# Kernel tuning notes

Hardware: AMD Instinct MI355X
Metric: run time of the kernel (lower is better)

The kernel has to match this reference:

```python
import jax, jax.numpy as jnp
import numpy as np

NUM_HEADS = 16
HEAD_DIM = 128
ROTARY_DIM = 32  # head_dim * rotary_pct(0.25)
ROPE_BASE = 10000.0
SCALE = HEAD_DIM ** -0.5


def _rotate_half(x):
    x1, x2 = jnp.split(x, 2, axis=-1)
    return jnp.concatenate((-x2, x1), axis=-1)


def _rope_tables(seq_len, dtype):
    inv_freq = 1.0 / (ROPE_BASE ** (jnp.arange(0, ROTARY_DIM, 2, dtype=jnp.float32) / ROTARY_DIM))
    freqs = jnp.arange(seq_len, dtype=jnp.float32)[:, None] * inv_freq[None, :]  # [S, rd/2]
    emb = jnp.concatenate((freqs, freqs), axis=-1)  # [S, rd]
    return jnp.cos(emb).astype(dtype), jnp.sin(emb).astype(dtype)


def setup_inputs() -> dict:
    key = jax.random.key(0)
    k1, k2, k3 = jax.random.split(key, 3)
    B, S, H = 2, 2048, 2048
    hidden_states = jax.random.normal(k1, (B, S, H), dtype=jnp.float32)
    attention_mask = jnp.zeros((B, 1, S, S), dtype=jnp.float32)
    Wqkv = jax.random.normal(k2, (H, 3 * H), dtype=jnp.float32) * (H ** -0.5)
    Wout = jax.random.normal(k3, (H, H), dtype=jnp.float32) * (H ** -0.5)
    return {"hidden_states": hidden_states, "attention_mask": attention_mask,
            "Wqkv": Wqkv, "Wout": Wout}


def reference(hidden_states, attention_mask, Wqkv, Wout):
    B, S, H = hidden_states.shape
    qkv = jnp.einsum('bsh,hk->bsk', hidden_states, Wqkv)  # [B,S,3H]
    q, k, v = jnp.split(qkv, 3, axis=-1)

    def to_heads(x):
        return x.reshape(B, S, NUM_HEADS, HEAD_DIM).transpose(0, 2, 1, 3)  # [B,nh,S,hd]

    q, k, v = to_heads(q), to_heads(k), to_heads(v)

    cos, sin = _rope_tables(S, hidden_states.dtype)  # [S, ROTARY_DIM]
    cos = cos[None, None, :, :]
    sin = sin[None, None, :, :]

    def rope(x):
        xr = x[..., :ROTARY_DIM]
        xr = xr * cos + _rotate_half(xr) * sin
        return jnp.concatenate((xr, x[..., ROTARY_DIM:]), axis=-1)

    q, k = rope(q), rope(k)

    scores = jnp.einsum('bhqd,bhkd->bhqk', q, k) * SCALE + attention_mask
    probs = jax.nn.softmax(scores, axis=-1)  # dropout p=0 -> identity
    ctx = jnp.einsum('bhqk,bhkd->bhqd', probs, v)
    ctx = ctx.transpose(0, 2, 1, 3).reshape(B, S, H)
    return jnp.einsum('bsh,ho->bso', ctx, Wout)
```

## Files before the change

### kernel.cpp

```cpp
#include <hip/hip_runtime.h>

typedef __attribute__((ext_vector_type(4))) float f32x4;
typedef __attribute__((ext_vector_type(8))) short s16x8;
typedef __attribute__((ext_vector_type(4))) unsigned short u16x4;
typedef __attribute__((ext_vector_type(8))) unsigned short u16x8;

#define DEVINL __device__ __forceinline__

constexpr int Bb = 2;
constexpr int Ss = 2048;
constexpr int Hh = 2048;
constexpr int NH = 16;
constexpr int HD = 128;
constexpr float ATT_SCALE = 0.08838834764831845f;
constexpr float CEXP = ATT_SCALE * 1.44269504089f;
constexpr float INV_SCALE = 11.313708498984761f;
constexpr float RAW_THR = 90.50966799f;

DEVINL unsigned short f2bf(float f) {
    unsigned u = __float_as_uint(f);
    u += 0x7FFFu + ((u >> 16) & 1u);
    return (unsigned short)(u >> 16);
}
DEVINL float bf2f(unsigned short h) { return __uint_as_float(((unsigned)h) << 16); }
DEVINL float fexp2(float x) { return __builtin_amdgcn_exp2f(x); }

DEVINL void gl16(const void* g, void* l) {
    __builtin_amdgcn_global_load_lds((const __attribute__((address_space(1))) void*)g,
                                     (__attribute__((address_space(3))) void*)l, 16, 0, 0);
}

__global__ void zero_flag_k(int* f) { if (threadIdx.x == 0) *f = 0; }

__global__ void scan_mask_k(const float* __restrict__ m, int* __restrict__ flag) {
    size_t i = ((size_t)blockIdx.x * 256 + threadIdx.x) * 4;
    f32x4 v = *(const f32x4*)(m + i);
    int any = (v[0] != 0.f) || (v[1] != 0.f) || (v[2] != 0.f) || (v[3] != 0.f);
    if (__any(any)) { if ((threadIdx.x & 63) == 0) atomicOr(flag, 1); }
}

__global__ void convH_k(const float* __restrict__ x, unsigned short* __restrict__ y) {
    size_t i = (size_t)blockIdx.x * 256 + threadIdx.x;
    f32x4 a = *(const f32x4*)(x + i * 8);
    f32x4 b = *(const f32x4*)(x + i * 8 + 4);
    u16x8 o;
    o[0] = f2bf(a[0]); o[1] = f2bf(a[1]); o[2] = f2bf(a[2]); o[3] = f2bf(a[3]);
    o[4] = f2bf(b[0]); o[5] = f2bf(b[1]); o[6] = f2bf(b[2]); o[7] = f2bf(b[3]);
    *(u16x8*)(y + i * 8) = o;
}

__global__ void convT_k(const float* __restrict__ W, unsigned short* __restrict__ Wt,
                        int R, int C) {
    __shared__ float tile[32][33];
    int c0 = blockIdx.x * 32, r0 = blockIdx.y * 32;
    int t = threadIdx.x;
    int rr = t >> 3, cc = (t & 7) * 4;
    f32x4 v = *(const f32x4*)(W + (size_t)(r0 + rr) * C + c0 + cc);
    tile[rr][cc + 0] = v[0]; tile[rr][cc + 1] = v[1];
    tile[rr][cc + 2] = v[2]; tile[rr][cc + 3] = v[3];
    __syncthreads();
    u16x4 o;
    o[0] = f2bf(tile[cc + 0][rr]); o[1] = f2bf(tile[cc + 1][rr]);
    o[2] = f2bf(tile[cc + 2][rr]); o[3] = f2bf(tile[cc + 3][rr]);
    *(u16x4*)(Wt + (size_t)(c0 + rr) * R + r0 + cc) = o;
}

#define PH(buf, kh, ih, sbuf, sunit, st, vm)                                      \
  {                                                                               \
    const char* Ar = lds + (buf)*65536;                                           \
    const char* Br = Ar + 32768;                                                  \
    s16x8 af[4];                                                                  \
    if ((ih) == 0) {                                                              \
      _Pragma("unroll")                                                           \
      for (int j = 0; j < 4; ++j) {                                               \
        int row = wn*64 + j*16 + lr;                                              \
        bfr[j] = *(const s16x8*)(Br + row*128 + (((kh)*64 + lg*16) ^ ((row&7)<<4))); \
      }                                                                           \
    }                                                                             \
    _Pragma("unroll")                                                             \
    for (int i = 0; i < 4; ++i) {                                                 \
      int row = wm*128 + (ih)*64 + i*16 + lr;                                     \
      af[i] = *(const s16x8*)(Ar + row*128 + (((kh)*64 + lg*16) ^ ((row&7)<<4))); \
    }                                                                             \
    STG(sbuf, sunit, st);                                                         \
    __builtin_amdgcn_s_barrier();                                                 \
    asm volatile("s_waitcnt lgkmcnt(0)" ::: "memory");                            \
    __builtin_amdgcn_s_setprio(1);                                                \
    _Pragma("unroll")                                                             \
    for (int i = 0; i < 4; ++i)                                                   \
      _Pragma("unroll")                                                           \
      for (int j = 0; j < 4; ++j)                                                 \
        acc[(ih)*4 + i][j] = __builtin_amdgcn_mfma_f32_16x16x32_bf16(             \
            af[i], bfr[j], acc[(ih)*4 + i][j], 0, 0, 0);                          \
    __builtin_amdgcn_s_setprio(0);                                                \
    if ((vm) == 2) { asm volatile("s_waitcnt vmcnt(2)" ::: "memory"); }           \
    if ((vm) == 4) { asm volatile("s_waitcnt vmcnt(4)" ::: "memory"); }           \
    __builtin_amdgcn_s_barrier();                                                 \
  }

template<int MODE>
__global__ __launch_bounds__(512, 2)
void gemm256_k(const unsigned short* __restrict__ A, const unsigned short* __restrict__ Bt,
               float* __restrict__ Cf, unsigned short* __restrict__ Cb,
               int M, int N, int K) {
    __shared__ char lds[131072];
    int t = threadIdx.x, w = t >> 6, ln = t & 63, lr = ln & 15, lg = ln >> 4;
    int wm = w >> 2, wn = w & 3;
    int f = blockIdx.x, cpx = gridDim.x >> 3;
    int s = (f & 7) * cpx + (f >> 3);
    int nbn = N >> 8;
    int nb = s % nbn, mb = s / nbn;
    int m0 = mb * 256, n0 = nb * 256;
    const char* Ab = (const char*)A;
    const char* Bbp = (const char*)Bt;

    f32x4 acc[8][4];
#pragma unroll
    for (int i = 0; i < 8; ++i)
#pragma unroll
        for (int j = 0; j < 4; ++j) { acc[i][j][0] = 0.f; acc[i][j][1] = 0.f; acc[i][j][2] = 0.f; acc[i][j][3] = 0.f; }

    auto STG = [&](int sbuf, int unit, int kt) {
        int isB = unit >> 1;
        const char* src = isB ? Bbp : Ab;
        int rbase = isB ? n0 : m0;
        char* reg = lds + sbuf * 65536 + isB * 32768;
        size_t kb = ((size_t)kt * 64) * 2;
#pragma unroll
        for (int rr = 0; rr < 2; ++rr) {
            int rowbase = isB ? ((unit & 1) * 128 + rr * 64)
                              : (rr * 128 + (unit & 1) * 64);
            int row = rowbase + (t >> 3);
            int slot = (t & 7) ^ (row & 7);
            gl16(src + ((size_t)(rbase + row) * K) * 2 + kb + slot * 16,
                 reg + rowbase * 128 + t * 16);
        }
    };

    const int NT = K >> 6;
    STG(0, 0, 0); STG(0, 2, 0); STG(0, 3, 0); STG(0, 1, 0);
    STG(1, 0, 1);
    asm volatile("s_waitcnt vmcnt(2)" ::: "memory");
    __builtin_amdgcn_s_barrier();

    s16x8 bfr[4];
    for (int it = 0; it < (NT >> 1); ++it) {
        int e = it * 2;
        int e2 = (e + 2 < NT) ? e + 2 : e;
        int e3 = (e + 3 < NT) ? e + 3 : e + 1;
        PH(0, 0, 0,  1, 2, e + 1, 4)
        PH(0, 0, 1,  1, 3, e + 1, -1)
        PH(0, 1, 0,  1, 1, e + 1, -1)
        PH(0, 1, 1,  0, 0, e2,    4)
        PH(1, 0, 0,  0, 2, e2,    4)
        PH(1, 0, 1,  0, 3, e2,   -1)
        PH(1, 1, 0,  0, 1, e2,   -1)
        PH(1, 1, 1,  1, 0, e3,    4)
    }
    asm volatile("s_waitcnt vmcnt(0)" ::: "memory");

    if (MODE == 0 && n0 < 4096 && (wn & 1) == 0) {
        float invf = fexp2((float)lr * -0.83048202372f);
#pragma unroll
        for (int i = 0; i < 8; ++i)
#pragma unroll
            for (int r = 0; r < 4; ++r) {
                int srow = (m0 + wm * 128 + i * 16 + lg * 4 + r) & (Ss - 1);
                float sn, cs;
                sincosf((float)srow * invf, &sn, &cs);
                float x1 = acc[i][0][r], x2 = acc[i][1][r];
                acc[i][0][r] = x1 * cs - x2 * sn;
                acc[i][1][r] = x2 * cs + x1 * sn;
            }
    }

#pragma unroll
    for (int i = 0; i < 8; ++i)
#pragma unroll
        for (int j = 0; j < 4; ++j)
#pragma unroll
            for (int r = 0; r < 4; ++r) {
                int gr = m0 + wm * 128 + i * 16 + lg * 4 + r;
                int gc = n0 + wn * 64 + j * 16 + lr;
                float vv = acc[i][j][r];
                if (MODE == 1) Cf[(size_t)gr * N + gc] = vv;
                else           Cb[(size_t)gr * N + gc] = f2bf(vv);
            }
}

template<int MODE>
__global__ __launch_bounds__(256)
void gemm_bt_k(const unsigned short* __restrict__ A, const unsigned short* __restrict__ Bt,
               float* __restrict__ Cf, unsigned short* __restrict__ Cb,
               int M, int N, int K) {
    __shared__ char lds[128 * 64 * 2 * 2];
    char* As = lds;
    char* Bs = lds + 128 * 64 * 2;
    int t = threadIdx.x, w = t >> 6, ln = t & 63, lr = ln & 15, lg = ln >> 4;
    int f = blockIdx.x;
    int cpx = gridDim.x >> 3;
    int s = (f & 7) * cpx + (f >> 3);
    int nbn = N >> 7;
    int nb = s % nbn, mb = s / nbn;
    int m0 = mb * 128, n0 = nb * 128;
    int wr = w >> 1, wc = w & 1;
    const char* Abt = (const char*)A;
    const char* Bbt = (const char*)Bt;

    f32x4 acc[4][4];
#pragma unroll
    for (int i = 0; i < 4; ++i)
#pragma unroll
        for (int j = 0; j < 4; ++j) { acc[i][j][0] = 0.f; acc[i][j][1] = 0.f; acc[i][j][2] = 0.f; acc[i][j][3] = 0.f; }

    for (int k0 = 0; k0 < K; k0 += 64) {
        __syncthreads();
#pragma unroll
        for (int vv = 0; vv < 4; ++vv) {
            int ci = vv * 256 + t;
            int row = ci >> 3, cb = (ci & 7) << 4;
            int sc = cb ^ ((row & 7) << 4);
            gl16(Abt + ((size_t)(m0 + row) * K + k0) * 2 + sc, As + ci * 16);
            gl16(Bbt + ((size_t)(n0 + row) * K + k0) * 2 + sc, Bs + ci * 16);
        }
        __syncthreads();
#pragma unroll
        for (int kc = 0; kc < 2; ++kc) {
            s16x8 af[4], bfr[4];
#pragma unroll
            for (int i = 0; i < 4; ++i) {
                int rowa = wr * 64 + i * 16 + lr;
                af[i] = *(const s16x8*)(As + rowa * 128 + ((kc * 64 + lg * 16) ^ ((rowa & 7) << 4)));
                int rowb = wc * 64 + i * 16 + lr;
                bfr[i] = *(const s16x8*)(Bs + rowb * 128 + ((kc * 64 + lg * 16) ^ ((rowb & 7) << 4)));
            }
#pragma unroll
            for (int i = 0; i < 4; ++i)
#pragma unroll
                for (int j = 0; j < 4; ++j)
                    acc[i][j] = __builtin_amdgcn_mfma_f32_16x16x32_bf16(af[i], bfr[j], acc[i][j], 0, 0, 0);
        }
    }
#pragma unroll
    for (int i = 0; i < 4; ++i)
#pragma unroll
        for (int j = 0; j < 4; ++j)
#pragma unroll
            for (int r = 0; r < 4; ++r) {
                int gr = m0 + wr * 64 + i * 16 + lg * 4 + r;
                int gc = n0 + wc * 64 + j * 16 + lr;
                float vv = acc[i][j][r];
                if (MODE == 1) Cf[(size_t)gr * N + gc] = vv;
                else           Cb[(size_t)gr * N + gc] = f2bf(vv);
            }
}

__global__ void vtrans_k(const unsigned short* __restrict__ qkv, unsigned short* __restrict__ Vt) {
    __shared__ unsigned short tile[64][40];
    int bh = blockIdx.x; int b = bh >> 4, h = bh & 15;
    int s0 = blockIdx.y * 64, d0 = blockIdx.z * 32;
    int t = threadIdx.x;
    int r = t >> 2, c8 = (t & 3) * 8;
    u16x8 v = *(const u16x8*)(qkv + ((size_t)(b * Ss + s0 + r)) * 6144 + 4096 + h * 128 + d0 + c8);
#pragma unroll
    for (int e = 0; e < 8; ++e) tile[r][c8 + e] = v[e];
    __syncthreads();
    int dr = t >> 3, sc = (t & 7) * 8;
    u16x8 o;
#pragma unroll
    for (int e = 0; e < 8; ++e) o[e] = tile[sc + e][dr];
    *(u16x8*)(Vt + ((size_t)bh * HD + d0 + dr) * Ss + s0 + sc) = o;
}

__global__ __launch_bounds__(512)
void attn_k(const unsigned short* __restrict__ qkv, const unsigned short* __restrict__ Vt,
            const float* __restrict__ mask, unsigned short* __restrict__ ctxb,
            const int* __restrict__ flag) {
    __shared__ char ldsK[2][16384];
    __shared__ char ldsV[2][16384];
    __shared__ unsigned short ldsP[8][1024];
    int f = blockIdx.x;
    int swzb = (f & 7) * 64 + (f >> 3);
    int bh = swzb >> 4, qt = swzb & 15;
    int b = bh >> 4, h = bh & 15;
    int t = threadIdx.x, w = t >> 6, ln = t & 63, lr = ln & 15, lg = ln >> 4;
    int useMask = *flag;
    int qw0 = qt * 128 + w * 16;
    const char* qkvB = (const char*)qkv;
    const char* VtB = (const char*)Vt;

    auto STAGE = [&](int buf, int kk0s) {
#pragma unroll
        for (int c = 0; c < 2; ++c) {
            int ci = c * 512 + t;
            int krow = ci >> 4, kcb = (ci & 15) << 4;
            gl16(qkvB + (((size_t)(b * Ss + kk0s + krow)) * 6144 + 2048 + h * 128) * 2 + (kcb ^ ((krow & 7) << 4)),
                 ldsK[buf] + ci * 16);
            int vrow = ci >> 3, vcb = (ci & 7) << 4;
            gl16(VtB + (((size_t)(bh * 128 + vrow)) * 2048 + kk0s) * 2 + (vcb ^ ((vrow & 7) << 4)),
                 ldsV[buf] + ci * 16);
        }
    };

    s16x8 qf[4];
    size_t qbase = ((size_t)(b * Ss + qw0 + lr)) * 6144 + h * 128;
#pragma unroll
    for (int kc = 0; kc < 4; ++kc) qf[kc] = *(const s16x8*)(qkv + qbase + kc * 32 + lg * 8);

    float mr = -3e38f, lsum = 0.f;
    f32x4 ctxa[8];
#pragma unroll
    for (int dn = 0; dn < 8; ++dn) { ctxa[dn][0] = 0.f; ctxa[dn][1] = 0.f; ctxa[dn][2] = 0.f; ctxa[dn][3] = 0.f; }
    const float* mrow = mask + (size_t)b * Ss * Ss;

    STAGE(0, 0);
    asm volatile("s_waitcnt vmcnt(0)" ::: "memory");
    __builtin_amdgcn_s_barrier();

    for (int tix = 0; tix < 32; ++tix) {
        int kk0 = tix * 64;
        int cur = tix & 1;
        if (kk0 + 64 < Ss) STAGE(cur ^ 1, kk0 + 64);

        f32x4 st[4];
#pragma unroll
        for (int n = 0; n < 4; ++n) {
            f32x4 sacc = {0.f, 0.f, 0.f, 0.f};
            const char* kb = ldsK[cur] + (n * 16 + lr) * 256;
            int sw = (lr & 7) << 4;
            s16x8 kf0 = *(const s16x8*)(kb + ((0 * 64 + lg * 16) ^ sw));
            s16x8 kf1 = *(const s16x8*)(kb + ((1 * 64 + lg * 16) ^ sw));
            s16x8 kf2 = *(const s16x8*)(kb + ((2 * 64 + lg * 16) ^ sw));
            s16x8 kf3 = *(const s16x8*)(kb + ((3 * 64 + lg * 16) ^ sw));
            __builtin_amdgcn_s_setprio(1);
            sacc = __builtin_amdgcn_mfma_f32_16x16x32_bf16(kf0, qf[0], sacc, 0, 0, 0);
            sacc = __builtin_amdgcn_mfma_f32_16x16x32_bf16(kf1, qf[1], sacc, 0, 0, 0);
            sacc = __builtin_amdgcn_mfma_f32_16x16x32_bf16(kf2, qf[2], sacc, 0, 0, 0);
            sacc = __builtin_amdgcn_mfma_f32_16x16x32_bf16(kf3, qf[3], sacc, 0, 0, 0);
            __builtin_amdgcn_s_setprio(0);
            st[n] = sacc;
        }
        if (useMask) {
#pragma unroll
            for (int n = 0; n < 4; ++n)
#pragma unroll
                for (int r = 0; r < 4; ++r)
                    st[n][r] += mrow[(size_t)(qw0 + lr) * Ss + kk0 + n * 16 + lg * 4 + r] * INV_SCALE;
        }
        float pmax = st[0][0];
#pragma unroll
        for (int n = 0; n < 4; ++n)
#pragma unroll
            for (int r = 0; r < 4; ++r) pmax = fmaxf(pmax, st[n][r]);
        pmax = fmaxf(pmax, __shfl_xor(pmax, 16));
        pmax = fmaxf(pmax, __shfl_xor(pmax, 32));
        bool need = pmax > mr + RAW_THR;
        if (__any(need)) {
            float mn = fmaxf(mr, pmax);
            float al = fexp2((mr - mn) * CEXP);
            mr = mn;
            lsum *= al;
            float a0 = __shfl(al, lg * 4 + 0), a1 = __shfl(al, lg * 4 + 1);
            float a2 = __shfl(al, lg * 4 + 2), a3 = __shfl(al, lg * 4 + 3);
#pragma unroll
            for (int dn = 0; dn < 8; ++dn) {
                ctxa[dn][0] *= a0; ctxa[dn][1] *= a1; ctxa[dn][2] *= a2; ctxa[dn][3] *= a3;
            }
        }
        float mC = mr * CEXP;
        float rs = 0.f;
        u16x4 pk[4];
#pragma unroll
        for (int n = 0; n < 4; ++n)
#pragma unroll
            for (int r = 0; r < 4; ++r) {
                float p = fexp2(st[n][r] * CEXP - mC);
                rs += p;
                pk[n][r] = f2bf(p);
            }
        rs += __shfl_xor(rs, 16);
        rs += __shfl_xor(rs, 32);
        lsum += rs;
        char* pw = (char*)ldsP[w];
        int swp = (lr & 7) << 4;
#pragma unroll
        for (int n = 0; n < 4; ++n)
            *(u16x4*)(pw + lr * 128 + ((32 * n + 8 * lg) ^ swp)) = pk[n];
        asm volatile("s_waitcnt lgkmcnt(0)" ::: "memory");
        s16x8 pa[2];
#pragma unroll
        for (int c2 = 0; c2 < 2; ++c2)
            pa[c2] = *(const s16x8*)(pw + lr * 128 + ((64 * c2 + 16 * lg) ^ swp));
#pragma unroll
        for (int dn = 0; dn < 8; ++dn) {
            const char* vb = ldsV[cur] + (dn * 16 + lr) * 128;
            s16x8 vf0 = *(const s16x8*)(vb + ((0 * 64 + lg * 16) ^ swp));
            s16x8 vf1 = *(const s16x8*)(vb + ((1 * 64 + lg * 16) ^ swp));
            __builtin_amdgcn_s_setprio(1);
            ctxa[dn] = __builtin_amdgcn_mfma_f32_16x16x32_bf16(pa[0], vf0, ctxa[dn], 0, 0, 0);
            ctxa[dn] = __builtin_amdgcn_mfma_f32_16x16x32_bf16(pa[1], vf1, ctxa[dn], 0, 0, 0);
            __builtin_amdgcn_s_setprio(0);
        }
        asm volatile("s_waitcnt vmcnt(0)" ::: "memory");
        __builtin_amdgcn_s_barrier();
    }
    float l0 = 1.f / __shfl(lsum, lg * 4 + 0), l1 = 1.f / __shfl(lsum, lg * 4 + 1);
    float l2 = 1.f / __shfl(lsum, lg * 4 + 2), l3 = 1.f / __shfl(lsum, lg * 4 + 3);
#pragma unroll
    for (int dn = 0; dn < 8; ++dn) {
        size_t base = ((size_t)(b * Ss + qw0)) * Hh + h * 128 + dn * 16 + lr;
        ctxb[base + (size_t)(lg * 4 + 0) * Hh] = f2bf(ctxa[dn][0] * l0);
        ctxb[base + (size_t)(lg * 4 + 1) * Hh] = f2bf(ctxa[dn][1] * l1);
        ctxb[base + (size_t)(lg * 4 + 2) * Hh] = f2bf(ctxa[dn][2] * l2);
        ctxb[base + (size_t)(lg * 4 + 3) * Hh] = f2bf(ctxa[dn][3] * l3);
    }
}

extern "C" void kernel_launch(void* const* d_in, const int* in_sizes, int n_in,
                              void* d_out, int out_size, void* d_ws, size_t ws_size,
                              hipStream_t stream) {
    (void)in_sizes; (void)n_in; (void)out_size; (void)ws_size;
    const float* hidden = (const float*)d_in[0];
    const float* mask   = (const float*)d_in[1];
    const float* Wqkv   = (const float*)d_in[2];
    const float* Wout   = (const float*)d_in[3];
    float* out = (float*)d_out;

    char* ws = (char*)d_ws;
    size_t off = 0;
    auto alloc = [&](size_t bytes) { char* p = ws + off; off += (bytes + 255) & ~(size_t)255; return p; };
    unsigned short* hbf   = (unsigned short*)alloc((size_t)8388608 * 2);
    unsigned short* wqkvT = (unsigned short*)alloc((size_t)12582912 * 2);
    unsigned short* woutT = (unsigned short*)alloc((size_t)4194304 * 2);
    unsigned short* qkv   = (unsigned short*)alloc((size_t)25165824 * 2);
    unsigned short* Vt    = (unsigned short*)alloc((size_t)8388608 * 2);
    int* flag             = (int*)alloc(256);
    unsigned short* ctx = hbf;

    zero_flag_k<<<1, 64, 0, stream>>>(flag);
    scan_mask_k<<<2048, 256, 0, stream>>>(mask, flag);
    convH_k<<<4096, 256, 0, stream>>>(hidden, hbf);
    convT_k<<<dim3(192, 64), 256, 0, stream>>>(Wqkv, wqkvT, 2048, 6144);
    convT_k<<<dim3(64, 64), 256, 0, stream>>>(Wout, woutT, 2048, 2048);
    gemm256_k<0><<<384, 512, 0, stream>>>(hbf, wqkvT, nullptr, qkv, 4096, 6144, 2048);
    vtrans_k<<<dim3(32, 32, 4), 256, 0, stream>>>(qkv, Vt);
    attn_k<<<512, 512, 0, stream>>>(qkv, Vt, mask, ctx, flag);
    gemm_bt_k<1><<<512, 256, 0, stream>>>(ctx, woutT, out, nullptr, 4096, 2048, 2048);
}
```

Measured before the change: 309.0 us.

## Replace both GEMMs with a pipelined 128x256-tile kernel using half-K LDS stages

Replaces the 256x256 QKV GEMM and the simple 128x128 output-projection GEMM with a single 128x256-tile kernel. Its LDS layout splits each K tile into 32-wide halves with a new XOR swizzle and keeps a double-buffered, barrier-phased prefetch schedule. The QKV GEMM now launches 768 blocks instead of 384, which improves occupancy and load balance on the many CUs, at the cost of less operand reuse per block. The output projection gains software pipelining but drops from 512 to 256 blocks.

```diff
diff --git a/kernel.cpp b/kernel.cpp
--- a/kernel.cpp
+++ b/kernel.cpp
@@ -65,24 +65,61 @@
     *(u16x4*)(Wt + (size_t)(c0 + rr) * R + r0 + cc) = o;
 }
 
-#define PH(buf, kh, ih, sbuf, sunit, st, vm)                                      \
+template<int MODE>
+__global__ __launch_bounds__(512, 2)
+void gemm128x256_k(const unsigned short* __restrict__ A, const unsigned short* __restrict__ Bt,
+                   float* __restrict__ Cf, unsigned short* __restrict__ Cb,
+                   int M, int N, int K) {
+    __shared__ char lds[98304];
+    int t = threadIdx.x, w = t >> 6, ln = t & 63, lr = ln & 15, lg = ln >> 4;
+    int wm = w >> 2, wn = w & 3;
+    int f = blockIdx.x, cpx = gridDim.x >> 3;
+    int s = (f & 7) * cpx + (f >> 3);
+    int nbn = N >> 8;
+    int nb = s % nbn, mb = s / nbn;
+    int m0 = mb * 128, n0 = nb * 256;
+    const char* Ab = (const char*)A;
+    const char* Bbp = (const char*)Bt;
+
+    f32x4 acc[4][4];
+#pragma unroll
+    for (int i = 0; i < 4; ++i)
+#pragma unroll
+        for (int j = 0; j < 4; ++j) { acc[i][j][0] = 0.f; acc[i][j][1] = 0.f; acc[i][j][2] = 0.f; acc[i][j][3] = 0.f; }
+
+    auto STGA = [&](int sbuf, int skh, int kt) {
+        int row = t >> 2, c = t & 3;
+        int cs = c ^ ((row >> 1) & 3);
+        gl16(Ab + ((size_t)(m0 + row) * K + kt * 64 + skh * 32) * 2 + cs * 16,
+             lds + sbuf * 49152 + skh * 8192 + t * 16);
+    };
+    auto STGB = [&](int sbuf, int skh, int kt) {
+#pragma unroll
+        for (int rr = 0; rr < 2; ++rr) {
+            int ci = rr * 512 + t;
+            int row = ci >> 2, c = ci & 3;
+            int cs = c ^ ((row >> 1) & 3);
+            gl16(Bbp + ((size_t)(n0 + row) * K + kt * 64 + skh * 32) * 2 + cs * 16,
+                 lds + sbuf * 49152 + 16384 + skh * 16384 + ci * 16);
+        }
+    };
+
+#define PH128(buf, kh, sbuf, skh, st)                                             \
   {                                                                               \
-    const char* Ar = lds + (buf)*65536;                                           \
-    const char* Br = Ar + 32768;                                                  \
-    s16x8 af[4];                                                                  \
-    if ((ih) == 0) {                                                              \
-      _Pragma("unroll")                                                           \
-      for (int j = 0; j < 4; ++j) {                                               \
-        int row = wn*64 + j*16 + lr;                                              \
-        bfr[j] = *(const s16x8*)(Br + row*128 + (((kh)*64 + lg*16) ^ ((row&7)<<4))); \
-      }                                                                           \
+    const char* Ap = lds + (buf) * 49152 + (kh) * 8192;                           \
+    const char* Bp = lds + (buf) * 49152 + 16384 + (kh) * 16384;                  \
+    s16x8 af[4], bfr[4];                                                          \
+    _Pragma("unroll")                                                             \
+    for (int i = 0; i < 4; ++i) {                                                 \
+      int row = wm * 64 + i * 16 + lr;                                            \
+      af[i] = *(const s16x8*)(Ap + row * 64 + ((lg ^ ((row >> 1) & 3)) * 16));    \
     }                                                                             \
     _Pragma("unroll")                                                             \
-    for (int i = 0; i < 4; ++i) {                                                 \
-      int row = wm*128 + (ih)*64 + i*16 + lr;                                     \
-      af[i] = *(const s16x8*)(Ar + row*128 + (((kh)*64 + lg*16) ^ ((row&7)<<4))); \
+    for (int j = 0; j < 4; ++j) {                                                 \
+      int row = wn * 64 + j * 16 + lr;                                            \
+      bfr[j] = *(const s16x8*)(Bp + row * 64 + ((lg ^ ((row >> 1) & 3)) * 16));   \
     }                                                                             \
-    STG(sbuf, sunit, st);                                                         \
+    STGA(sbuf, skh, st); STGB(sbuf, skh, st);                                     \
     __builtin_amdgcn_s_barrier();                                                 \
     asm volatile("s_waitcnt lgkmcnt(0)" ::: "memory");                            \
     __builtin_amdgcn_s_setprio(1);                                                \
@@ -90,82 +127,39 @@
     for (int i = 0; i < 4; ++i)                                                   \
       _Pragma("unroll")                                                           \
       for (int j = 0; j < 4; ++j)                                                 \
-        acc[(ih)*4 + i][j] = __builtin_amdgcn_mfma_f32_16x16x32_bf16(             \
-            af[i], bfr[j], acc[(ih)*4 + i][j], 0, 0, 0);                          \
+        acc[i][j] = __builtin_amdgcn_mfma_f32_16x16x32_bf16(af[i], bfr[j],        \
+                                                            acc[i][j], 0, 0, 0); \
     __builtin_amdgcn_s_setprio(0);                                                \
-    if ((vm) == 2) { asm volatile("s_waitcnt vmcnt(2)" ::: "memory"); }           \
-    if ((vm) == 4) { asm volatile("s_waitcnt vmcnt(4)" ::: "memory"); }           \
+    asm volatile("s_waitcnt vmcnt(6)" ::: "memory");                              \
     __builtin_amdgcn_s_barrier();                                                 \
   }
 
-template<int MODE>
-__global__ __launch_bounds__(512, 2)
-void gemm256_k(const unsigned short* __restrict__ A, const unsigned short* __restrict__ Bt,
-               float* __restrict__ Cf, unsigned short* __restrict__ Cb,
-               int M, int N, int K) {
-    __shared__ char lds[131072];
-    int t = threadIdx.x, w = t >> 6, ln = t & 63, lr = ln & 15, lg = ln >> 4;
-    int wm = w >> 2, wn = w & 3;
-    int f = blockIdx.x, cpx = gridDim.x >> 3;
-    int s = (f & 7) * cpx + (f >> 3);
-    int nbn = N >> 8;
-    int nb = s % nbn, mb = s / nbn;
-    int m0 = mb * 256, n0 = nb * 256;
-    const char* Ab = (const char*)A;
-    const char* Bbp = (const char*)Bt;
-
-    f32x4 acc[8][4];
-#pragma unroll
-    for (int i = 0; i < 8; ++i)
-#pragma unroll
-        for (int j = 0; j < 4; ++j) { acc[i][j][0] = 0.f; acc[i][j][1] = 0.f; acc[i][j][2] = 0.f; acc[i][j][3] = 0.f; }
-
-    auto STG = [&](int sbuf, int unit, int kt) {
-        int isB = unit >> 1;
-        const char* src = isB ? Bbp : Ab;
-        int rbase = isB ? n0 : m0;
-        char* reg = lds + sbuf * 65536 + isB * 32768;
-        size_t kb = ((size_t)kt * 64) * 2;
-#pragma unroll
-        for (int rr = 0; rr < 2; ++rr) {
-            int rowbase = isB ? ((unit & 1) * 128 + rr * 64)
-                              : (rr * 128 + (unit & 1) * 64);
-            int row = rowbase + (t >> 3);
-            int slot = (t & 7) ^ (row & 7);
-            gl16(src + ((size_t)(rbase + row) * K) * 2 + kb + slot * 16,
-                 reg + rowbase * 128 + t * 16);
-        }
-    };
-
     const int NT = K >> 6;
-    STG(0, 0, 0); STG(0, 2, 0); STG(0, 3, 0); STG(0, 1, 0);
-    STG(1, 0, 1);
-    asm volatile("s_waitcnt vmcnt(2)" ::: "memory");
+    STGA(0, 0, 0); STGB(0, 0, 0);
+    STGA(0, 1, 0); STGB(0, 1, 0);
+    STGA(1, 0, 1); STGB(1, 0, 1);
+    asm volatile("s_waitcnt vmcnt(3)" ::: "memory");
     __builtin_amdgcn_s_barrier();
 
-    s16x8 bfr[4];
     for (int it = 0; it < (NT >> 1); ++it) {
         int e = it * 2;
         int e2 = (e + 2 < NT) ? e + 2 : e;
         int e3 = (e + 3 < NT) ? e + 3 : e + 1;
-        PH(0, 0, 0,  1, 2, e + 1, 4)
-        PH(0, 0, 1,  1, 3, e + 1, -1)
-        PH(0, 1, 0,  1, 1, e + 1, -1)
-        PH(0, 1, 1,  0, 0, e2,    4)
-        PH(1, 0, 0,  0, 2, e2,    4)
-        PH(1, 0, 1,  0, 3, e2,   -1)
-        PH(1, 1, 0,  0, 1, e2,   -1)
-        PH(1, 1, 1,  1, 0, e3,    4)
+        PH128(0, 0,  1, 1, e + 1)
+        PH128(0, 1,  0, 0, e2)
+        PH128(1, 0,  0, 1, e2)
+        PH128(1, 1,  1, 0, e3)
     }
     asm volatile("s_waitcnt vmcnt(0)" ::: "memory");
+#undef PH128
 
     if (MODE == 0 && n0 < 4096 && (wn & 1) == 0) {
         float invf = fexp2((float)lr * -0.83048202372f);
 #pragma unroll
-        for (int i = 0; i < 8; ++i)
+        for (int i = 0; i < 4; ++i)
 #pragma unroll
             for (int r = 0; r < 4; ++r) {
-                int srow = (m0 + wm * 128 + i * 16 + lg * 4 + r) & (Ss - 1);
+                int srow = (m0 + wm * 64 + i * 16 + lg * 4 + r) & (Ss - 1);
                 float sn, cs;
                 sincosf((float)srow * invf, &sn, &cs);
                 float x1 = acc[i][0][r], x2 = acc[i][1][r];
@@ -175,80 +169,13 @@
     }
 
 #pragma unroll
-    for (int i = 0; i < 8; ++i)
+    for (int i = 0; i < 4; ++i)
 #pragma unroll
         for (int j = 0; j < 4; ++j)
 #pragma unroll
             for (int r = 0; r < 4; ++r) {
-                int gr = m0 + wm * 128 + i * 16 + lg * 4 + r;
+                int gr = m0 + wm * 64 + i * 16 + lg * 4 + r;
                 int gc = n0 + wn * 64 + j * 16 + lr;
-                float vv = acc[i][j][r];
-                if (MODE == 1) Cf[(size_t)gr * N + gc] = vv;
-                else           Cb[(size_t)gr * N + gc] = f2bf(vv);
-            }
-}
-
-template<int MODE>
-__global__ __launch_bounds__(256)
-void gemm_bt_k(const unsigned short* __restrict__ A, const unsigned short* __restrict__ Bt,
-               float* __restrict__ Cf, unsigned short* __restrict__ Cb,
-               int M, int N, int K) {
-    __shared__ char lds[128 * 64 * 2 * 2];
-    char* As = lds;
-    char* Bs = lds + 128 * 64 * 2;
-    int t = threadIdx.x, w = t >> 6, ln = t & 63, lr = ln & 15, lg = ln >> 4;
-    int f = blockIdx.x;
-    int cpx = gridDim.x >> 3;
-    int s = (f & 7) * cpx + (f >> 3);
-    int nbn = N >> 7;
-    int nb = s % nbn, mb = s / nbn;
-    int m0 = mb * 128, n0 = nb * 128;
-    int wr = w >> 1, wc = w & 1;
-    const char* Abt = (const char*)A;
-    const char* Bbt = (const char*)Bt;
-
-    f32x4 acc[4][4];
-#pragma unroll
-    for (int i = 0; i < 4; ++i)
-#pragma unroll
-        for (int j = 0; j < 4; ++j) { acc[i][j][0] = 0.f; acc[i][j][1] = 0.f; acc[i][j][2] = 0.f; acc[i][j][3] = 0.f; }
-
-    for (int k0 = 0; k0 < K; k0 += 64) {
-        __syncthreads();
-#pragma unroll
-        for (int vv = 0; vv < 4; ++vv) {
-            int ci = vv * 256 + t;
-            int row = ci >> 3, cb = (ci & 7) << 4;
-            int sc = cb ^ ((row & 7) << 4);
-            gl16(Abt + ((size_t)(m0 + row) * K + k0) * 2 + sc, As + ci * 16);
-            gl16(Bbt + ((size_t)(n0 + row) * K + k0) * 2 + sc, Bs + ci * 16);
-        }
-        __syncthreads();
-#pragma unroll
-        for (int kc = 0; kc < 2; ++kc) {
-            s16x8 af[4], bfr[4];
-#pragma unroll
-            for (int i = 0; i < 4; ++i) {
-                int rowa = wr * 64 + i * 16 + lr;
-                af[i] = *(const s16x8*)(As + rowa * 128 + ((kc * 64 + lg * 16) ^ ((rowa & 7) << 4)));
-                int rowb = wc * 64 + i * 16 + lr;
-                bfr[i] = *(const s16x8*)(Bs + rowb * 128 + ((kc * 64 + lg * 16) ^ ((rowb & 7) << 4)));
-            }
-#pragma unroll
-            for (int i = 0; i < 4; ++i)
-#pragma unroll
-                for (int j = 0; j < 4; ++j)
-                    acc[i][j] = __builtin_amdgcn_mfma_f32_16x16x32_bf16(af[i], bfr[j], acc[i][j], 0, 0, 0);
-        }
-    }
-#pragma unroll
-    for (int i = 0; i < 4; ++i)
-#pragma unroll
-        for (int j = 0; j < 4; ++j)
-#pragma unroll
-            for (int r = 0; r < 4; ++r) {
-                int gr = m0 + wr * 64 + i * 16 + lg * 4 + r;
-                int gc = n0 + wc * 64 + j * 16 + lr;
                 float vv = acc[i][j][r];
                 if (MODE == 1) Cf[(size_t)gr * N + gc] = vv;
                 else           Cb[(size_t)gr * N + gc] = f2bf(vv);
@@ -442,8 +369,8 @@
     convH_k<<<4096, 256, 0, stream>>>(hidden, hbf);
     convT_k<<<dim3(192, 64), 256, 0, stream>>>(Wqkv, wqkvT, 2048, 6144);
     convT_k<<<dim3(64, 64), 256, 0, stream>>>(Wout, woutT, 2048, 2048);
-    gemm256_k<0><<<384, 512, 0, stream>>>(hbf, wqkvT, nullptr, qkv, 4096, 6144, 2048);
+    gemm128x256_k<0><<<768, 512, 0, stream>>>(hbf, wqkvT, nullptr, qkv, 4096, 6144, 2048);
     vtrans_k<<<dim3(32, 32, 4), 256, 0, stream>>>(qkv, Vt);
     attn_k<<<512, 512, 0, stream>>>(qkv, Vt, mask, ctx, flag);
-    gemm_bt_k<1><<<512, 256, 0, stream>>>(ctx, woutT, out, nullptr, 4096, 2048, 2048);
-}
+    gemm128x256_k<1><<<256, 512, 0, stream>>>(ctx, woutT, out, nullptr, 4096, 2048, 2048);
+}
```

Result: faster. 301.6 us (-2.4%).
